# Kernel optimization log

Measured on AMD Instinct MI355X. Metric: run time of the kernel, lower is better.

## Reference

```python
import jax, jax.numpy as jnp
import numpy as np

QK_DIM = 64
V_DIM = 64
NUM_Q_HEADS = 16
NUM_KV_HEADS = 4
GROUP = NUM_Q_HEADS // NUM_KV_HEADS
SCALE = 1.0 / (QK_DIM ** 0.5)


def setup_inputs() -> dict:
    key = jax.random.key(0)
    kq, kk, kv = jax.random.split(key, 3)
    B, S = 2, 2048
    Q = jax.random.normal(kq, (B, S, NUM_Q_HEADS * QK_DIM), dtype=jnp.float32)
    K = jax.random.normal(kk, (B, S, NUM_KV_HEADS * QK_DIM), dtype=jnp.float32)
    V = jax.random.normal(kv, (B, S, NUM_KV_HEADS * V_DIM), dtype=jnp.float32)
    # causal mask, [B, 1, S, S]; 0 entries are masked (matches masked_fill(mask == 0, -inf))
    mask = jnp.broadcast_to(jnp.tril(jnp.ones((S, S), dtype=jnp.int32))[None, None], (B, 1, S, S))
    return {"Q": Q, "K": K, "V": V, "mask": mask}


def reference(Q, K, V, mask):
    B, S, _ = Q.shape
    # [B, Hkv, g, S, d]
    Qg = Q.reshape(B, S, NUM_Q_HEADS, QK_DIM).transpose(0, 2, 1, 3).reshape(B, NUM_KV_HEADS, GROUP, S, QK_DIM)
    Kh = K.reshape(B, S, NUM_KV_HEADS, QK_DIM).transpose(0, 2, 1, 3)  # [B, Hkv, S, d]
    Vh = V.reshape(B, S, NUM_KV_HEADS, V_DIM).transpose(0, 2, 1, 3)   # [B, Hkv, S, dv]
    # scores: [B, Hkv, g, S, S]
    scores = jnp.einsum('bhgsd,bhtd->bhgst', Qg, Kh) * SCALE
    scores = jnp.where(mask[:, None] == 0, -jnp.inf, scores)
    probs = jax.nn.softmax(scores, axis=-1)
    # dropout p=0.0 -> identity (eval semantics)
    out = jnp.einsum('bhgst,bhtv->bhgsv', probs, Vh)
    return out
```

## Files before the change

### kernel.cpp

```cpp
#include <hip/hip_runtime.h>
#include <hip/hip_bf16.h>

typedef unsigned short u16;
typedef unsigned int u32;
typedef __attribute__((ext_vector_type(8))) short bf16x8;
typedef __attribute__((ext_vector_type(16))) float f32x16;

#define S_LEN 2048
#define NHQ   16
#define NHKV  4
#define HD    64
#define KVBLK 64
#define LPAD  72
#define MOPAD 68
#define KVSTR (NHKV*HD)
#define QSTR  (NHQ*HD)
#define QSCALE 0.18033688011112042f
#define DEFER_THR 8.0f

__device__ __forceinline__ u32 cvt2(float lo, float hi) {
    __hip_bfloat162 hh = __float22bfloat162_rn(make_float2(lo, hi));
    union { __hip_bfloat162 h; u32 u; } c; c.h = hh; return c.u;
}
__device__ __forceinline__ u16 cvt1(float x) {
    __hip_bfloat16 hh = __float2bfloat16(x);
    union { __hip_bfloat16 h; u16 u; } c; c.h = hh; return c.u;
}

__global__ __launch_bounds__(512, 2)
void gqa_fwd_kernel(const float* __restrict__ Qp, const float* __restrict__ Kp,
                    const float* __restrict__ Vp, float* __restrict__ Op)
{
    __shared__ __align__(16) u16 Kl[2][KVBLK][LPAD];
    __shared__ __align__(16) u16 Vt[2][HD][LPAD];
    __shared__ __align__(16) float Mo[4][32][MOPAD];
    __shared__ float Mm[4][32], Ml[4][32];

    const int tid  = threadIdx.x;
    const int w    = tid >> 6;
    const int lane = tid & 63;
    const int q31  = lane & 31;
    const int h    = lane >> 5;

    const int g   = __popc(w) & 1;
    const int rg  = w >> 1;
    const int sid = rg * 64 + lane;

    const int bid  = blockIdx.x;
    const int head = bid & 31;
    const int j    = bid >> 5;
    const int kvh  = head & 3;
    const int b    = (head >> 2) & 1;
    const int qh   = kvh * 4 + (head >> 3);

    const float* Kbase = Kp + (size_t)b * S_LEN * KVSTR + kvh*HD;
    const float* Vbase = Vp + (size_t)b * S_LEN * KVSTR + kvh*HD;
    const float* Qhead = Qp + (size_t)b * S_LEN * QSTR + qh*HD;
    float*       Ohead = Op + (size_t)(b*NHQ + qh) * S_LEN * HD;

    const int krow = sid >> 2;
    const int kd   = (sid & 3) * 16;
    const int vrow = sid & 63;
    const int vd0  = (sid >> 6) * 16;

    float4 kpf[4], vpf[4];

    auto ISSUE = [&](int tt) {
        const float* kp = Kbase + (size_t)(tt*KVBLK + krow)*KVSTR + kd;
        const float* vp = Vbase + (size_t)(tt*KVBLK + vrow)*KVSTR + vd0;
        kpf[0] = *(const float4*)(kp);
        kpf[1] = *(const float4*)(kp + 4);
        kpf[2] = *(const float4*)(kp + 8);
        kpf[3] = *(const float4*)(kp + 12);
        vpf[0] = *(const float4*)(vp);
        vpf[1] = *(const float4*)(vp + 4);
        vpf[2] = *(const float4*)(vp + 8);
        vpf[3] = *(const float4*)(vp + 12);
        asm volatile("" ::: "memory");
    };
    auto WRITE = [&](int tt) {
        const int bf = tt & 1;
        *(uint4*)(&Kl[bf][krow][kd]) = make_uint4(
            cvt2(kpf[0].x,kpf[0].y), cvt2(kpf[0].z,kpf[0].w),
            cvt2(kpf[1].x,kpf[1].y), cvt2(kpf[1].z,kpf[1].w));
        *(uint4*)(&Kl[bf][krow][kd+8]) = make_uint4(
            cvt2(kpf[2].x,kpf[2].y), cvt2(kpf[2].z,kpf[2].w),
            cvt2(kpf[3].x,kpf[3].y), cvt2(kpf[3].z,kpf[3].w));
        #pragma unroll
        for (int ii = 0; ii < 4; ++ii) {
            Vt[bf][vd0+4*ii+0][vrow] = cvt1(vpf[ii].x);
            Vt[bf][vd0+4*ii+1][vrow] = cvt1(vpf[ii].y);
            Vt[bf][vd0+4*ii+2][vrow] = cvt1(vpf[ii].z);
            Vt[bf][vd0+4*ii+3][vrow] = cvt1(vpf[ii].w);
        }
    };

    #pragma unroll 1
    for (int pass = 0; pass < 2; ++pass) {
        const int qt = pass ? j : (15 - j);
        const int nt = 2*qt + 1;
        const int dr = rg >> 1;
        const int my_tmax = 2*qt + ((dr == g) ? dr : dr - 1);
        const int diagw   = 2*qt + dr;
        const int qcmp    = q31 + 32*(rg & 1);
        const int qrow    = qt*128 + rg*32 + q31;

        bf16x8 qf[4];
        {
            const float* qp = Qhead + (size_t)qrow * QSTR;
            #pragma unroll
            for (int ks = 0; ks < 4; ++ks) {
                const int d = ks*16 + h*8;
                const float4 x = *(const float4*)(qp + d);
                const float4 y = *(const float4*)(qp + d + 4);
                union { u32 u[4]; bf16x8 v; } t4;
                t4.u[0] = cvt2(x.x*QSCALE, x.y*QSCALE);
                t4.u[1] = cvt2(x.z*QSCALE, x.w*QSCALE);
                t4.u[2] = cvt2(y.x*QSCALE, y.y*QSCALE);
                t4.u[3] = cvt2(y.z*QSCALE, y.w*QSCALE);
                qf[ks] = t4.v;
            }
        }

        f32x16 oacc0, oacc1;
        #pragma unroll
        for (int i = 0; i < 16; ++i) { oacc0[i] = 0.f; oacc1[i] = 0.f; }
        float m_s = -1e30f, l_p = 0.f;

        if (g == 0) { ISSUE(0); WRITE(0); if (nt >= 2) ISSUE(2); }
        else        { ISSUE(1); }
        __syncthreads();

        for (int t = 0; t <= nt; ++t) {
            if ((t & 1) == g) {
                if (t <= my_tmax) {
                    const int bf = t & 1;
                    f32x16 s0, s1;
                    #pragma unroll
                    for (int i = 0; i < 16; ++i) { s0[i] = 0.f; s1[i] = 0.f; }
                    __builtin_amdgcn_s_setprio(1);
                    #pragma unroll
                    for (int ks = 0; ks < 4; ++ks) {
                        bf16x8 k0 = *(const bf16x8*)(&Kl[bf][q31][ks*16 + h*8]);
                        bf16x8 k1 = *(const bf16x8*)(&Kl[bf][32 + q31][ks*16 + h*8]);
                        s0 = __builtin_amdgcn_mfma_f32_32x32x16_bf16(k0, qf[ks], s0, 0, 0, 0);
                        s1 = __builtin_amdgcn_mfma_f32_32x32x16_bf16(k1, qf[ks], s1, 0, 0, 0);
                    }
                    __builtin_amdgcn_s_setprio(0);

                    if (t == diagw) {
                        #pragma unroll
                        for (int rgi = 0; rgi < 16; ++rgi) {
                            const int kvl = (rgi & 3) + 8*(rgi >> 2) + 4*h;
                            if (kvl > qcmp)      s0[rgi] = -1e30f;
                            if (kvl + 32 > qcmp) s1[rgi] = -1e30f;
                        }
                    }

                    float mx[8];
                    #pragma unroll
                    for (int i = 0; i < 8; ++i)
                        mx[i] = fmaxf(fmaxf(s0[i], s0[i+8]), fmaxf(s1[i], s1[i+8]));
                    const float lmax = fmaxf(fmaxf(fmaxf(mx[0],mx[1]), fmaxf(mx[2],mx[3])),
                                             fmaxf(fmaxf(mx[4],mx[5]), fmaxf(mx[6],mx[7])));

                    if (!__all(lmax <= m_s + DEFER_THR)) {
                        float rmax = fmaxf(lmax, __shfl_xor(lmax, 32));
                        const float mnew = fmaxf(m_s, rmax);
                        const float cf   = __builtin_amdgcn_exp2f(m_s - mnew);
                        m_s = mnew;
                        l_p *= cf;
                        #pragma unroll
                        for (int i = 0; i < 16; ++i) { oacc0[i] *= cf; oacc1[i] *= cf; }
                    }

                    float ps0 = 0.f, ps1 = 0.f;
                    #pragma unroll
                    for (int rgi = 0; rgi < 16; ++rgi) {
                        const float p0 = __builtin_amdgcn_exp2f(s0[rgi] - m_s);
                        const float p1 = __builtin_amdgcn_exp2f(s1[rgi] - m_s);
                        s0[rgi] = p0; ps0 += p0;
                        s1[rgi] = p1; ps1 += p1;
                    }
                    l_p += ps0 + ps1;

                    u32 Aw[8], Bw[8];
                    #pragma unroll
                    for (int m = 0; m < 4; ++m) {
                        Aw[m]   = cvt2(s0[m*4+0], s0[m*4+1]);
                        Bw[m]   = cvt2(s0[m*4+2], s0[m*4+3]);
                        Aw[4+m] = cvt2(s1[m*4+0], s1[m*4+1]);
                        Bw[4+m] = cvt2(s1[m*4+2], s1[m*4+3]);
                    }

                    __builtin_amdgcn_s_setprio(1);
                    #pragma unroll
                    for (int c = 0; c < 4; ++c) {
                        u32 w0 = Aw[2*c], w2 = Aw[2*c+1];
                        u32 w1 = Bw[2*c], w3 = Bw[2*c+1];
                        asm("v_permlane32_swap_b32 %0, %1" : "+v"(w0), "+v"(w2));
                        asm("v_permlane32_swap_b32 %0, %1" : "+v"(w1), "+v"(w3));
                        union { u32 u[4]; bf16x8 v; } pu;
                        pu.u[0] = w0; pu.u[1] = w1; pu.u[2] = w2; pu.u[3] = w3;
                        bf16x8 v0 = *(const bf16x8*)(&Vt[bf][q31][c*16 + h*8]);
                        bf16x8 v1 = *(const bf16x8*)(&Vt[bf][32 + q31][c*16 + h*8]);
                        oacc0 = __builtin_amdgcn_mfma_f32_32x32x16_bf16(v0, pu.v, oacc0, 0, 0, 0);
                        oacc1 = __builtin_amdgcn_mfma_f32_32x32x16_bf16(v1, pu.v, oacc1, 0, 0, 0);
                    }
                    __builtin_amdgcn_s_setprio(0);
                }
            } else {
                if (t + 1 <= nt) WRITE(t + 1);
                if (t + 3 <= nt) ISSUE(t + 3);
            }
            __syncthreads();
        }

        l_p += __shfl_xor(l_p, 32);
        if (g == 1) {
            #pragma unroll
            for (int k2 = 0; k2 < 4; ++k2) {
                *(float4*)(&Mo[rg][q31][8*k2 + 4*h]) =
                    make_float4(oacc0[4*k2], oacc0[4*k2+1], oacc0[4*k2+2], oacc0[4*k2+3]);
                *(float4*)(&Mo[rg][q31][32 + 8*k2 + 4*h]) =
                    make_float4(oacc1[4*k2], oacc1[4*k2+1], oacc1[4*k2+2], oacc1[4*k2+3]);
            }
            if (h == 0) { Mm[rg][q31] = m_s; Ml[rg][q31] = l_p; }
        }
        __syncthreads();
        if (g == 0) {
            const float m1 = Mm[rg][q31], l1 = Ml[rg][q31];
            const float mn  = fmaxf(m_s, m1);
            const float a   = __builtin_amdgcn_exp2f(m_s - mn);
            const float bsc = __builtin_amdgcn_exp2f(m1 - mn);
            const float inv = 1.0f / (a*l_p + bsc*l1);
            const float ai = a*inv, bi = bsc*inv;
            float* ob = Ohead + (size_t)qrow * HD;
            #pragma unroll
            for (int k2 = 0; k2 < 4; ++k2) {
                const float4 p0 = *(const float4*)(&Mo[rg][q31][8*k2 + 4*h]);
                const float4 p1 = *(const float4*)(&Mo[rg][q31][32 + 8*k2 + 4*h]);
                float4 o;
                o.x = oacc0[4*k2+0]*ai + p0.x*bi;
                o.y = oacc0[4*k2+1]*ai + p0.y*bi;
                o.z = oacc0[4*k2+2]*ai + p0.z*bi;
                o.w = oacc0[4*k2+3]*ai + p0.w*bi;
                *(float4*)(ob + 8*k2 + 4*h) = o;
                o.x = oacc1[4*k2+0]*ai + p1.x*bi;
                o.y = oacc1[4*k2+1]*ai + p1.y*bi;
                o.z = oacc1[4*k2+2]*ai + p1.z*bi;
                o.w = oacc1[4*k2+3]*ai + p1.w*bi;
                *(float4*)(ob + 32 + 8*k2 + 4*h) = o;
            }
        }
    }
}

extern "C" void kernel_launch(void* const* d_in, const int* in_sizes, int n_in,
                              void* d_out, int out_size, void* d_ws, size_t ws_size,
                              hipStream_t stream) {
    const float* Q = (const float*)d_in[0];
    const float* K = (const float*)d_in[1];
    const float* V = (const float*)d_in[2];
    float* O = (float*)d_out;
    gqa_fwd_kernel<<<dim3(256), dim3(512), 0, stream>>>(Q, K, V, O);
}
```

Baseline: 49.43 us.

## Give each wave group its own double-buffered K/V tiles and process tiles concurrently

Previously the two wave groups alternated: one computed on a shared KV tile while the other loaded the next one, so each group sat idle half the time. Now each group owns a private double-buffered K/V region in LDS and loads its own tiles (even or odd). Both groups compute every iteration, with the next tile's global loads issued before the compute and written to LDS after it. This roughly halves the iteration count and barrier count, but doubles K/V LDS use, which may hurt occupancy. Every wave now does load, convert and transpose work in each step, and a barrier is added at the end of each pass.

New measurement: 54.12 us. +9.5%, slower.

```diff
diff --git a/kernel.cpp b/kernel.cpp
--- a/kernel.cpp
+++ b/kernel.cpp
@@ -31,8 +31,8 @@
 void gqa_fwd_kernel(const float* __restrict__ Qp, const float* __restrict__ Kp,
                     const float* __restrict__ Vp, float* __restrict__ Op)
 {
-    __shared__ __align__(16) u16 Kl[2][KVBLK][LPAD];
-    __shared__ __align__(16) u16 Vt[2][HD][LPAD];
+    __shared__ __align__(16) u16 Kl[2][2][KVBLK][LPAD];
+    __shared__ __align__(16) u16 Vt[2][2][HD][LPAD];
     __shared__ __align__(16) float Mo[4][32][MOPAD];
     __shared__ float Mm[4][32], Ml[4][32];
 
@@ -79,31 +79,29 @@
         asm volatile("" ::: "memory");
     };
     auto WRITE = [&](int tt) {
-        const int bf = tt & 1;
-        *(uint4*)(&Kl[bf][krow][kd]) = make_uint4(
+        const int bf = (tt >> 1) & 1;
+        *(uint4*)(&Kl[g][bf][krow][kd]) = make_uint4(
             cvt2(kpf[0].x,kpf[0].y), cvt2(kpf[0].z,kpf[0].w),
             cvt2(kpf[1].x,kpf[1].y), cvt2(kpf[1].z,kpf[1].w));
-        *(uint4*)(&Kl[bf][krow][kd+8]) = make_uint4(
+        *(uint4*)(&Kl[g][bf][krow][kd+8]) = make_uint4(
             cvt2(kpf[2].x,kpf[2].y), cvt2(kpf[2].z,kpf[2].w),
             cvt2(kpf[3].x,kpf[3].y), cvt2(kpf[3].z,kpf[3].w));
         #pragma unroll
         for (int ii = 0; ii < 4; ++ii) {
-            Vt[bf][vd0+4*ii+0][vrow] = cvt1(vpf[ii].x);
-            Vt[bf][vd0+4*ii+1][vrow] = cvt1(vpf[ii].y);
-            Vt[bf][vd0+4*ii+2][vrow] = cvt1(vpf[ii].z);
-            Vt[bf][vd0+4*ii+3][vrow] = cvt1(vpf[ii].w);
+            Vt[g][bf][vd0+4*ii+0][vrow] = cvt1(vpf[ii].x);
+            Vt[g][bf][vd0+4*ii+1][vrow] = cvt1(vpf[ii].y);
+            Vt[g][bf][vd0+4*ii+2][vrow] = cvt1(vpf[ii].z);
+            Vt[g][bf][vd0+4*ii+3][vrow] = cvt1(vpf[ii].w);
         }
     };
 
     #pragma unroll 1
     for (int pass = 0; pass < 2; ++pass) {
         const int qt = pass ? j : (15 - j);
-        const int nt = 2*qt + 1;
-        const int dr = rg >> 1;
-        const int my_tmax = 2*qt + ((dr == g) ? dr : dr - 1);
-        const int diagw   = 2*qt + dr;
-        const int qcmp    = q31 + 32*(rg & 1);
-        const int qrow    = qt*128 + rg*32 + q31;
+        const int dr    = rg >> 1;
+        const int tmax  = 2*qt + dr;
+        const int qcmp  = q31 + 32*(rg & 1);
+        const int qrow  = qt*128 + rg*32 + q31;
 
         bf16x8 qf[4];
         {
@@ -127,92 +125,93 @@
         for (int i = 0; i < 16; ++i) { oacc0[i] = 0.f; oacc1[i] = 0.f; }
         float m_s = -1e30f, l_p = 0.f;
 
-        if (g == 0) { ISSUE(0); WRITE(0); if (nt >= 2) ISSUE(2); }
-        else        { ISSUE(1); }
+        ISSUE(g);
+        WRITE(g);
         __syncthreads();
 
-        for (int t = 0; t <= nt; ++t) {
-            if ((t & 1) == g) {
-                if (t <= my_tmax) {
-                    const int bf = t & 1;
-                    f32x16 s0, s1;
-                    #pragma unroll
-                    for (int i = 0; i < 16; ++i) { s0[i] = 0.f; s1[i] = 0.f; }
-                    __builtin_amdgcn_s_setprio(1);
-                    #pragma unroll
-                    for (int ks = 0; ks < 4; ++ks) {
-                        bf16x8 k0 = *(const bf16x8*)(&Kl[bf][q31][ks*16 + h*8]);
-                        bf16x8 k1 = *(const bf16x8*)(&Kl[bf][32 + q31][ks*16 + h*8]);
-                        s0 = __builtin_amdgcn_mfma_f32_32x32x16_bf16(k0, qf[ks], s0, 0, 0, 0);
-                        s1 = __builtin_amdgcn_mfma_f32_32x32x16_bf16(k1, qf[ks], s1, 0, 0, 0);
-                    }
-                    __builtin_amdgcn_s_setprio(0);
-
-                    if (t == diagw) {
-                        #pragma unroll
-                        for (int rgi = 0; rgi < 16; ++rgi) {
-                            const int kvl = (rgi & 3) + 8*(rgi >> 2) + 4*h;
-                            if (kvl > qcmp)      s0[rgi] = -1e30f;
-                            if (kvl + 32 > qcmp) s1[rgi] = -1e30f;
-                        }
-                    }
-
-                    float mx[8];
-                    #pragma unroll
-                    for (int i = 0; i < 8; ++i)
-                        mx[i] = fmaxf(fmaxf(s0[i], s0[i+8]), fmaxf(s1[i], s1[i+8]));
-                    const float lmax = fmaxf(fmaxf(fmaxf(mx[0],mx[1]), fmaxf(mx[2],mx[3])),
-                                             fmaxf(fmaxf(mx[4],mx[5]), fmaxf(mx[6],mx[7])));
-
-                    if (!__all(lmax <= m_s + DEFER_THR)) {
-                        float rmax = fmaxf(lmax, __shfl_xor(lmax, 32));
-                        const float mnew = fmaxf(m_s, rmax);
-                        const float cf   = __builtin_amdgcn_exp2f(m_s - mnew);
-                        m_s = mnew;
-                        l_p *= cf;
-                        #pragma unroll
-                        for (int i = 0; i < 16; ++i) { oacc0[i] *= cf; oacc1[i] *= cf; }
-                    }
-
-                    float ps0 = 0.f, ps1 = 0.f;
+        for (int p = 0; p <= qt; ++p) {
+            const int t    = 2*p + g;
+            const bool more = (p + 1 <= qt);
+            if (more) ISSUE(t + 2);
+
+            if (t <= tmax) {
+                const int bf = p & 1;
+                f32x16 s0, s1;
+                #pragma unroll
+                for (int i = 0; i < 16; ++i) { s0[i] = 0.f; s1[i] = 0.f; }
+                __builtin_amdgcn_s_setprio(1);
+                #pragma unroll
+                for (int ks = 0; ks < 4; ++ks) {
+                    bf16x8 k0 = *(const bf16x8*)(&Kl[g][bf][q31][ks*16 + h*8]);
+                    bf16x8 k1 = *(const bf16x8*)(&Kl[g][bf][32 + q31][ks*16 + h*8]);
+                    s0 = __builtin_amdgcn_mfma_f32_32x32x16_bf16(k0, qf[ks], s0, 0, 0, 0);
+                    s1 = __builtin_amdgcn_mfma_f32_32x32x16_bf16(k1, qf[ks], s1, 0, 0, 0);
+                }
+                __builtin_amdgcn_s_setprio(0);
+
+                if (t == tmax) {
                     #pragma unroll
                     for (int rgi = 0; rgi < 16; ++rgi) {
-                        const float p0 = __builtin_amdgcn_exp2f(s0[rgi] - m_s);
-                        const float p1 = __builtin_amdgcn_exp2f(s1[rgi] - m_s);
-                        s0[rgi] = p0; ps0 += p0;
-                        s1[rgi] = p1; ps1 += p1;
+                        const int kvl = (rgi & 3) + 8*(rgi >> 2) + 4*h;
+                        if (kvl > qcmp)      s0[rgi] = -1e30f;
+                        if (kvl + 32 > qcmp) s1[rgi] = -1e30f;
                     }
-                    l_p += ps0 + ps1;
-
-                    u32 Aw[8], Bw[8];
+                }
+
+                float mx[8];
+                #pragma unroll
+                for (int i = 0; i < 8; ++i)
+                    mx[i] = fmaxf(fmaxf(s0[i], s0[i+8]), fmaxf(s1[i], s1[i+8]));
+                const float lmax = fmaxf(fmaxf(fmaxf(mx[0],mx[1]), fmaxf(mx[2],mx[3])),
+                                         fmaxf(fmaxf(mx[4],mx[5]), fmaxf(mx[6],mx[7])));
+
+                if (!__all(lmax <= m_s + DEFER_THR)) {
+                    float rmax = fmaxf(lmax, __shfl_xor(lmax, 32));
+                    const float mnew = fmaxf(m_s, rmax);
+                    const float cf   = __builtin_amdgcn_exp2f(m_s - mnew);
+                    m_s = mnew;
+                    l_p *= cf;
                     #pragma unroll
-                    for (int m = 0; m < 4; ++m) {
-                        Aw[m]   = cvt2(s0[m*4+0], s0[m*4+1]);
-                        Bw[m]   = cvt2(s0[m*4+2], s0[m*4+3]);
-                        Aw[4+m] = cvt2(s1[m*4+0], s1[m*4+1]);
-                        Bw[4+m] = cvt2(s1[m*4+2], s1[m*4+3]);
-                    }
-
-                    __builtin_amdgcn_s_setprio(1);
-                    #pragma unroll
-                    for (int c = 0; c < 4; ++c) {
-                        u32 w0 = Aw[2*c], w2 = Aw[2*c+1];
-                        u32 w1 = Bw[2*c], w3 = Bw[2*c+1];
-                        asm("v_permlane32_swap_b32 %0, %1" : "+v"(w0), "+v"(w2));
-                        asm("v_permlane32_swap_b32 %0, %1" : "+v"(w1), "+v"(w3));
-                        union { u32 u[4]; bf16x8 v; } pu;
-                        pu.u[0] = w0; pu.u[1] = w1; pu.u[2] = w2; pu.u[3] = w3;
-                        bf16x8 v0 = *(const bf16x8*)(&Vt[bf][q31][c*16 + h*8]);
-                        bf16x8 v1 = *(const bf16x8*)(&Vt[bf][32 + q31][c*16 + h*8]);
-                        oacc0 = __builtin_amdgcn_mfma_f32_32x32x16_bf16(v0, pu.v, oacc0, 0, 0, 0);
-                        oacc1 = __builtin_amdgcn_mfma_f32_32x32x16_bf16(v1, pu.v, oacc1, 0, 0, 0);
-                    }
-                    __builtin_amdgcn_s_setprio(0);
-                }
-            } else {
-                if (t + 1 <= nt) WRITE(t + 1);
-                if (t + 3 <= nt) ISSUE(t + 3);
-            }
+                    for (int i = 0; i < 16; ++i) { oacc0[i] *= cf; oacc1[i] *= cf; }
+                }
+
+                float ps0 = 0.f, ps1 = 0.f;
+                #pragma unroll
+                for (int rgi = 0; rgi < 16; ++rgi) {
+                    const float p0 = __builtin_amdgcn_exp2f(s0[rgi] - m_s);
+                    const float p1 = __builtin_amdgcn_exp2f(s1[rgi] - m_s);
+                    s0[rgi] = p0; ps0 += p0;
+                    s1[rgi] = p1; ps1 += p1;
+                }
+                l_p += ps0 + ps1;
+
+                u32 Aw[8], Bw[8];
+                #pragma unroll
+                for (int m = 0; m < 4; ++m) {
+                    Aw[m]   = cvt2(s0[m*4+0], s0[m*4+1]);
+                    Bw[m]   = cvt2(s0[m*4+2], s0[m*4+3]);
+                    Aw[4+m] = cvt2(s1[m*4+0], s1[m*4+1]);
+                    Bw[4+m] = cvt2(s1[m*4+2], s1[m*4+3]);
+                }
+
+                __builtin_amdgcn_s_setprio(1);
+                #pragma unroll
+                for (int c = 0; c < 4; ++c) {
+                    u32 w0 = Aw[2*c], w2 = Aw[2*c+1];
+                    u32 w1 = Bw[2*c], w3 = Bw[2*c+1];
+                    asm("v_permlane32_swap_b32 %0, %1" : "+v"(w0), "+v"(w2));
+                    asm("v_permlane32_swap_b32 %0, %1" : "+v"(w1), "+v"(w3));
+                    union { u32 u[4]; bf16x8 v; } pu;
+                    pu.u[0] = w0; pu.u[1] = w1; pu.u[2] = w2; pu.u[3] = w3;
+                    bf16x8 v0 = *(const bf16x8*)(&Vt[g][bf][q31][c*16 + h*8]);
+                    bf16x8 v1 = *(const bf16x8*)(&Vt[g][bf][32 + q31][c*16 + h*8]);
+                    oacc0 = __builtin_amdgcn_mfma_f32_32x32x16_bf16(v0, pu.v, oacc0, 0, 0, 0);
+                    oacc1 = __builtin_amdgcn_mfma_f32_32x32x16_bf16(v1, pu.v, oacc1, 0, 0, 0);
+                }
+                __builtin_amdgcn_s_setprio(0);
+            }
+
+            if (more) WRITE(t + 2);
             __syncthreads();
         }
 
@@ -253,6 +252,7 @@
                 *(float4*)(ob + 32 + 8*k2 + 4*h) = o;
             }
         }
+        __syncthreads();
     }
 }
 
```
